# Performance work log

Hardware: AMD Instinct MI355X
Metric: run time of the kernel (lower is better)

Reference implementation:

```python
import jax, jax.numpy as jnp
import numpy as np

N_NODES = 100000
N_EDGES = 1600000
IN_CH, HID_CH, OUT_CH = 128, 128, 64


def _glorot(key, shape):
    lim = np.sqrt(6.0 / (shape[0] + shape[1])).astype(np.float32)
    return jax.random.uniform(key, shape, jnp.float32, -lim, lim)


def setup_inputs() -> dict:
    key = jax.random.key(0)
    ks = jax.random.split(key, 11)
    x = jax.random.normal(ks[0], (N_NODES, IN_CH), jnp.float32)
    edge_index = jax.random.randint(ks[1], (2, N_EDGES), 0, N_NODES, dtype=jnp.int64)
    dims = [(IN_CH, HID_CH), (HID_CH, HID_CH), (HID_CH, OUT_CH)]
    params = {}
    for i, (din, dout) in enumerate(dims):
        params[f"Wl{i}"] = _glorot(ks[2 + 3 * i], (din, dout))
        params[f"Wr{i}"] = _glorot(ks[3 + 3 * i], (din, dout))
        params[f"b{i}"] = jnp.zeros((dout,), jnp.float32)
    return {"x": x, "edge_index": edge_index, **params}


def _sage_conv(x, src, dst, Wl, Wr, b):
    # mean aggregation of neighbor (source) features at each destination node
    msg_sum = jax.ops.segment_sum(x[src], dst, num_segments=N_NODES)  # [N, din]
    deg = jax.ops.segment_sum(jnp.ones((src.shape[0],), x.dtype), dst,
                              num_segments=N_NODES)
    mean = msg_sum / jnp.maximum(deg, 1.0)[:, None]
    # lin_l(aggr) + lin_r(self), bias only in lin_l (PyG SAGEConv default)
    return mean @ Wl + x @ Wr + b


def reference(x, edge_index, Wl0, Wr0, b0, Wl1, Wr1, b1, Wl2, Wr2, b2):
    src, dst = edge_index[0], edge_index[1]
    h = jax.nn.relu(_sage_conv(x, src, dst, Wl0, Wr0, b0))  # dropout = identity (eval)
    h = jax.nn.relu(_sage_conv(h, src, dst, Wl1, Wr1, b1))
    out = _sage_conv(h, src, dst, Wl2, Wr2, b2)
    return out
```

## Files before the change

### kernel.cpp

```cpp
#include <hip/hip_runtime.h>
#include <stdint.h>

#define NN 100000
#define NE 1600000
#define NBUK 782
#define G 256
#define CHUNK 6250

typedef unsigned int u32;
typedef unsigned short u16;
typedef short v8s __attribute__((ext_vector_type(8)));
typedef float v4f __attribute__((ext_vector_type(4)));

union U4S8 {
    uint4 u;
    v8s s;
};

__device__ __forceinline__ float bf2f(u16 u) {
    return __uint_as_float(((u32)u) << 16);
}
__device__ __forceinline__ u16 f2bf(float f) {
    u32 u = __float_as_uint(f);
    u = u + 0x7FFFu + ((u >> 16) & 1u);
    return (u16)(u >> 16);
}
__device__ __forceinline__ float lo16(u32 u) { return __uint_as_float(u << 16); }
__device__ __forceinline__ float hi16(u32 u) {
    return __uint_as_float(u & 0xFFFF0000u);
}

__global__ void detect_kernel(const u32* __restrict__ ei,
                              const u32* __restrict__ x, int* flags) {
    __shared__ int bad64, badbf;
    int t = threadIdx.x;
    if (t == 0) { bad64 = 0; badbf = 0; }
    __syncthreads();
    if (ei[2 * t + 1] != 0u) atomicAdd(&bad64, 1);
    u32 d = x[t];
    u32 e = (d >> 7) & 0xFFu;
    if (e != 0u && (e < 96u || e > 160u)) atomicAdd(&badbf, 1);
    __syncthreads();
    if (t == 0) {
        flags[0] = (bad64 < 16) ? 1 : 0;
        flags[1] = (badbf < 16) ? 1 : 0;
    }
}

__global__ void conv_x(const void* __restrict__ x, const int* __restrict__ flags,
                       u32* __restrict__ xb, u32* __restrict__ h1,
                       u32* __restrict__ h2) {
    int i = blockIdx.x * 256 + threadIdx.x;
    if (i >= NN * 64) {
        int p = i - NN * 64;
        if (p < 64) {
            xb[NN * 64 + p] = 0;
            h1[NN * 64 + p] = 0;
            h2[NN * 64 + p] = 0;
        }
        return;
    }
    u32 o;
    if (flags[1]) {
        o = ((const u32*)x)[i];
    } else {
        float2 v = ((const float2*)x)[i];
        o = ((u32)f2bf(v.y) << 16) | (u32)f2bf(v.x);
    }
    xb[i] = o;
}

__global__ void wt_prep_all(const void* __restrict__ Wr0,
                            const void* __restrict__ Wl0,
                            const void* __restrict__ b0,
                            const void* __restrict__ Wr1,
                            const void* __restrict__ Wl1,
                            const void* __restrict__ b1,
                            const void* __restrict__ Wr2,
                            const void* __restrict__ Wl2,
                            const void* __restrict__ b2,
                            const int* __restrict__ flags,
                            u16* __restrict__ WT0, float* __restrict__ bf0,
                            u16* __restrict__ WT1, float* __restrict__ bf1,
                            u16* __restrict__ WT2, float* __restrict__ bf2_) {
    const void* Wr;
    const void* Wl;
    const void* bias;
    u16* WT;
    float* bias_f;
    int cout, t;
    if (blockIdx.x < 128) {
        Wr = Wr0; Wl = Wl0; bias = b0; WT = WT0; bias_f = bf0; cout = 128;
        t = blockIdx.x * 256 + threadIdx.x;
    } else if (blockIdx.x < 256) {
        Wr = Wr1; Wl = Wl1; bias = b1; WT = WT1; bias_f = bf1; cout = 128;
        t = (blockIdx.x - 128) * 256 + threadIdx.x;
    } else {
        Wr = Wr2; Wl = Wl2; bias = b2; WT = WT2; bias_f = bf2_; cout = 64;
        t = (blockIdx.x - 256) * 256 + threadIdx.x;
    }
    if (t < 256 * cout) {
        int k = t / cout, c = t % cout;
        const void* W = (k < 128) ? Wr : Wl;
        int kk = k & 127;
        float v;
        if (flags[1])
            v = bf2f(((const u16*)W)[kk * cout + c]);
        else
            v = ((const float*)W)[kk * cout + c];
        WT[c * 256 + k] = f2bf(v);
    }
    if (t < cout) {
        bias_f[t] =
            flags[1] ? bf2f(((const u16*)bias)[t]) : ((const float*)bias)[t];
    }
}

__global__ __launch_bounds__(256) void p1_hist(const void* __restrict__ ei,
                                               const int* __restrict__ flags,
                                               int* __restrict__ hist) {
    __shared__ int h[NBUK];
    int g = blockIdx.x, t = threadIdx.x;
    for (int b = t; b < NBUK; b += 256) h[b] = 0;
    __syncthreads();
    int e0 = g * CHUNK;
    int e1 = e0 + CHUNK;
    const int* p = (const int*)ei;
    if (flags[0]) {
        for (int e = e0 + t; e < e1; e += 256)
            atomicAdd(&h[p[2 * (NE + e)] >> 7], 1);
    } else {
        for (int e = e0 + t; e < e1; e += 256)
            atomicAdd(&h[p[NE + e] >> 7], 1);
    }
    __syncthreads();
    for (int b = t; b < NBUK; b += 256) hist[b * G + g] = h[b];
}

__global__ void scan_block_g(const int* __restrict__ in, int* __restrict__ out,
                             int* __restrict__ bsums, int n) {
    __shared__ int sS[256];
    int t = threadIdx.x;
    int base = blockIdx.x * 1024 + t * 4;
    int c[4];
#pragma unroll
    for (int i = 0; i < 4; ++i) c[i] = (base + i < n) ? in[base + i] : 0;
    int s = c[0] + c[1] + c[2] + c[3];
    sS[t] = s;
    __syncthreads();
    for (int dlt = 1; dlt < 256; dlt <<= 1) {
        int v = (t >= dlt) ? sS[t - dlt] : 0;
        __syncthreads();
        sS[t] += v;
        __syncthreads();
    }
    int run = sS[t] - s;
    if (t == 255) bsums[blockIdx.x] = sS[255];
#pragma unroll
    for (int i = 0; i < 4; ++i) {
        if (base + i < n) out[base + i] = run;
        run += c[i];
    }
}

__global__ void scan_top_g(int* bsums, int nb) {
    __shared__ int sS[256];
    int t = threadIdx.x;
    int v = (t < nb) ? bsums[t] : 0;
    sS[t] = v;
    __syncthreads();
    for (int d = 1; d < 256; d <<= 1) {
        int u = (t >= d) ? sS[t - d] : 0;
        __syncthreads();
        sS[t] += u;
        __syncthreads();
    }
    if (t < nb) bsums[t] = sS[t] - v;
}

__global__ void scan_add_g(int* __restrict__ out, const int* __restrict__ bsums,
                           int n) {
    int i = blockIdx.x * 256 + threadIdx.x;
    if (i < n) out[i] += bsums[i >> 10];
}

__global__ __launch_bounds__(256) void p2_scatter(const void* __restrict__ ei,
                                                  const int* __restrict__ flags,
                                                  const int* __restrict__ histS,
                                                  int2* __restrict__ ebuf) {
    __shared__ int cur[NBUK];
    int g = blockIdx.x, t = threadIdx.x;
    for (int b = t; b < NBUK; b += 256) cur[b] = histS[b * G + g];
    __syncthreads();
    int e0 = g * CHUNK;
    int e1 = e0 + CHUNK;
    const int* p = (const int*)ei;
    int is64 = flags[0];
    for (int e = e0 + t; e < e1; e += 256) {
        int s, d;
        if (is64) {
            s = p[2 * e];
            d = p[2 * (NE + e)];
        } else {
            s = p[e];
            d = p[NE + e];
        }
        int pos = atomicAdd(&cur[d >> 7], 1);
        ebuf[pos] = make_int2(s, d);
    }
}

__global__ __launch_bounds__(256) void p3_build(const int* __restrict__ histS,
                                                const int2* __restrict__ ebuf,
                                                int* __restrict__ off,
                                                int* __restrict__ ssrc) {
    __shared__ int cnt[128], pref[128], cur[128];
    int b = blockIdx.x, t = threadIdx.x;
    int node0 = b << 7;
    int bs = histS[b * G];
    int be = (b == NBUK - 1) ? NE : histS[(b + 1) * G];
    if (t < 128) cnt[t] = 0;
    __syncthreads();
    for (int e = bs + t; e < be; e += 256)
        atomicAdd(&cnt[ebuf[e].y - node0], 1);
    __syncthreads();
    if (t < 128) pref[t] = cnt[t];
    __syncthreads();
    for (int d = 1; d < 128; d <<= 1) {
        int v = 0;
        if (t < 128 && t >= d) v = pref[t - d];
        __syncthreads();
        if (t < 128) pref[t] += v;
        __syncthreads();
    }
    if (t < 128) {
        int ex = pref[t] - cnt[t];
        cur[t] = ex;
        int node = node0 + t;
        if (node < NN) off[node] = bs + ex;
    }
    if (b == NBUK - 1 && t == 0) off[NN] = NE;
    __syncthreads();
    for (int e = bs + t; e < be; e += 256) {
        int2 sd = ebuf[e];
        int pos = atomicAdd(&cur[sd.y - node0], 1);
        ssrc[bs + pos] = sd.x;
    }
}

__global__ __launch_bounds__(256) void gather_mean_b(
    const u32* __restrict__ feat, const int* __restrict__ off,
    const int* __restrict__ ssrc, u32* __restrict__ meanB) {
    int node = blockIdx.x * 4 + (threadIdx.x >> 6);
    int lane = threadIdx.x & 63;
    int o0 = __builtin_amdgcn_readfirstlane(off[node]);
    int o1 = __builtin_amdgcn_readfirstlane(off[node + 1]);
    int cnt = o1 - o0;
    float a0 = 0.f, a1 = 0.f;
    for (int base = 0; base < cnt; base += 64) {
        int lim = cnt - base;
        if (lim > 64) lim = 64;
        int myidx = (lane < lim) ? ssrc[o0 + base + lane] : NN;
        int jb = (lim + 15) & ~15;
        for (int j = 0; j < jb; j += 16) {
            u32 uu[16];
#pragma unroll
            for (int q = 0; q < 16; ++q) {
                int sidx = __builtin_amdgcn_readlane(myidx, j + q);
                uu[q] = feat[(size_t)sidx * 64 + lane];
            }
#pragma unroll
            for (int q = 0; q < 16; ++q) {
                a0 += lo16(uu[q]);
                a1 += hi16(uu[q]);
            }
        }
    }
    float inv = 1.0f / (float)(cnt > 0 ? cnt : 1);
    meanB[node * 64 + lane] =
        ((u32)f2bf(a1 * inv) << 16) | (u32)f2bf(a0 * inv);
}

template <int COUT, bool RELU, bool FINAL>
__global__ __launch_bounds__(256) void sage_mfma(
    const u16* __restrict__ selfB, const u16* __restrict__ meanB,
    const u16* __restrict__ WT, const float* __restrict__ bias_f,
    void* __restrict__ out, const int* __restrict__ flags) {
    constexpr int NT = COUT / 16;
    const int tid = threadIdx.x;
    const int wave = tid >> 6;
    const int lane = tid & 63;
    const int n16 = lane & 15;
    const int quad = lane >> 4;
    const int rowbase = blockIdx.x * 128 + wave * 32;
    const int bfin = flags[1];

    int ar0 = rowbase + n16;
    int ar1 = rowbase + 16 + n16;
    ar0 = (ar0 < NN) ? ar0 : (NN - 1);
    ar1 = (ar1 < NN) ? ar1 : (NN - 1);

    const u16* aS0 = selfB + (size_t)ar0 * 128 + quad * 8;
    const u16* aS1 = selfB + (size_t)ar1 * 128 + quad * 8;
    const u16* aM0 = meanB + (size_t)ar0 * 128 + quad * 8;
    const u16* aM1 = meanB + (size_t)ar1 * 128 + quad * 8;
    const u16* bp = WT + (size_t)n16 * 256 + quad * 8;

    v4f acc[2][NT];
#pragma unroll
    for (int mt = 0; mt < 2; ++mt)
#pragma unroll
        for (int nt = 0; nt < NT; ++nt) acc[mt][nt] = (v4f)(0.f);

#pragma unroll
    for (int ks = 0; ks < 8; ++ks) {
        const int ko = (ks & 3) * 32;
        U4S8 a0, a1;
        a0.u = *(const uint4*)((ks < 4 ? aS0 : aM0) + ko);
        a1.u = *(const uint4*)((ks < 4 ? aS1 : aM1) + ko);
        U4S8 b[NT];
#pragma unroll
        for (int nt = 0; nt < NT; ++nt)
            b[nt].u = *(const uint4*)(bp + nt * 16 * 256 + ks * 32);
#pragma unroll
        for (int nt = 0; nt < NT; ++nt) {
            acc[0][nt] = __builtin_amdgcn_mfma_f32_16x16x32_bf16(
                a0.s, b[nt].s, acc[0][nt], 0, 0, 0);
            acc[1][nt] = __builtin_amdgcn_mfma_f32_16x16x32_bf16(
                a1.s, b[nt].s, acc[1][nt], 0, 0, 0);
        }
    }

#pragma unroll
    for (int nt = 0; nt < NT; ++nt) {
        const int c = nt * 16 + n16;
        const float bv = bias_f[c];
#pragma unroll
        for (int mt = 0; mt < 2; ++mt) {
#pragma unroll
            for (int r = 0; r < 4; ++r) {
                int row = rowbase + mt * 16 + quad * 4 + r;
                if (row < NN) {
                    float v = acc[mt][nt][r] + bv;
                    if (RELU) v = fmaxf(v, 0.f);
                    if (FINAL && !bfin)
                        ((float*)out)[(size_t)row * COUT + c] = v;
                    else
                        ((u16*)out)[(size_t)row * COUT + c] = f2bf(v);
                }
            }
        }
    }
}

extern "C" void kernel_launch(void* const* d_in, const int* in_sizes, int n_in,
                              void* d_out, int out_size, void* d_ws,
                              size_t ws_size, hipStream_t stream) {
    const void* x = d_in[0];
    const void* ei = d_in[1];
    const void* Wl0 = d_in[2];
    const void* Wr0 = d_in[3];
    const void* b0 = d_in[4];
    const void* Wl1 = d_in[5];
    const void* Wr1 = d_in[6];
    const void* b1 = d_in[7];
    const void* Wl2 = d_in[8];
    const void* Wr2 = d_in[9];
    const void* b2 = d_in[10];

    char* ws = (char*)d_ws;
    size_t o = 0;
    auto alloc = [&](size_t bytes) {
        void* p = ws + o;
        o = (o + bytes + 511) & ~(size_t)511;
        return p;
    };
    int* flags = (int*)alloc(16);
    int* hist = (int*)alloc((size_t)NBUK * G * 4);
    int* bsums = (int*)alloc(256 * 4);
    int* off = (int*)alloc((NN + 1) * 4);
    int* ssrc = (int*)alloc((size_t)NE * 4);
    int2* ebuf = (int2*)alloc((size_t)NE * 8);
    u32* xb = (u32*)alloc((size_t)(NN + 1) * 64 * 4);
    u32* meanB = (u32*)alloc((size_t)NN * 64 * 4);
    u32* h1 = (u32*)alloc((size_t)(NN + 1) * 64 * 4);
    u32* h2 = (u32*)alloc((size_t)(NN + 1) * 64 * 4);
    u16* WT0 = (u16*)alloc(256 * 128 * 2);
    u16* WT1 = (u16*)alloc(256 * 128 * 2);
    u16* WT2 = (u16*)alloc(256 * 64 * 2);
    float* bf0 = (float*)alloc(128 * 4);
    float* bf1 = (float*)alloc(128 * 4);
    float* bf2_ = (float*)alloc(64 * 4);

    constexpr int L = NBUK * G;
    constexpr int NBLK = (L + 1023) / 1024;
    constexpr int RB = (NN + 127) / 128;

    detect_kernel<<<1, 256, 0, stream>>>((const u32*)ei, (const u32*)x, flags);
    conv_x<<<(NN * 64 + 64 + 255) / 256, 256, 0, stream>>>(x, flags, xb, h1,
                                                           h2);
    wt_prep_all<<<320, 256, 0, stream>>>(Wr0, Wl0, b0, Wr1, Wl1, b1, Wr2, Wl2,
                                         b2, flags, WT0, bf0, WT1, bf1, WT2,
                                         bf2_);

    p1_hist<<<G, 256, 0, stream>>>(ei, flags, hist);
    scan_block_g<<<NBLK, 256, 0, stream>>>(hist, hist, bsums, L);
    scan_top_g<<<1, 256, 0, stream>>>(bsums, NBLK);
    scan_add_g<<<(L + 255) / 256, 256, 0, stream>>>(hist, bsums, L);
    p2_scatter<<<G, 256, 0, stream>>>(ei, flags, hist, ebuf);
    p3_build<<<NBUK, 256, 0, stream>>>(hist, ebuf, off, ssrc);

    gather_mean_b<<<NN / 4, 256, 0, stream>>>(xb, off, ssrc, meanB);
    sage_mfma<128, true, false><<<RB, 256, 0, stream>>>(
        (const u16*)xb, (const u16*)meanB, WT0, bf0, h1, flags);
    gather_mean_b<<<NN / 4, 256, 0, stream>>>(h1, off, ssrc, meanB);
    sage_mfma<128, true, false><<<RB, 256, 0, stream>>>(
        (const u16*)h1, (const u16*)meanB, WT1, bf1, h2, flags);
    gather_mean_b<<<NN / 4, 256, 0, stream>>>(h2, off, ssrc, meanB);
    sage_mfma<64, false, true><<<RB, 256, 0, stream>>>(
        (const u16*)h2, (const u16*)meanB, WT2, bf2_, d_out, flags);
}
```

Baseline: 481.4 us.

## Stage weights in swizzled LDS and tile 64 rows per wave in SAGE MFMA

The SAGE linear kernel now copies the transposed weight matrix into shared memory with an XOR swizzle once per block. Each wave then computes 64 rows instead of 32, and the MFMA operands are swapped so outputs come out row-contiguous. That allows vectorized float4/uint2 stores with the bias loaded as float4. The aim is to cut repeated global weight loads and scattered scalar stores, at the cost of 64KB of LDS per block, which limits occupancy, and more accumulator registers.

```diff
diff --git a/kernel.cpp b/kernel.cpp
--- a/kernel.cpp
+++ b/kernel.cpp
@@ -282,71 +282,103 @@
 }
 
 template <int COUT, bool RELU, bool FINAL>
-__global__ __launch_bounds__(256) void sage_mfma(
+__global__ __launch_bounds__(256, 2) void sage_mfma(
     const u16* __restrict__ selfB, const u16* __restrict__ meanB,
     const u16* __restrict__ WT, const float* __restrict__ bias_f,
     void* __restrict__ out, const int* __restrict__ flags) {
-    constexpr int NT = COUT / 16;
+    constexpr int CT = COUT / 16;
+    __shared__ u16 wlds[256 * COUT];
     const int tid = threadIdx.x;
     const int wave = tid >> 6;
     const int lane = tid & 63;
     const int n16 = lane & 15;
     const int quad = lane >> 4;
-    const int rowbase = blockIdx.x * 128 + wave * 32;
     const int bfin = flags[1];
 
-    int ar0 = rowbase + n16;
-    int ar1 = rowbase + 16 + n16;
-    ar0 = (ar0 < NN) ? ar0 : (NN - 1);
-    ar1 = (ar1 < NN) ? ar1 : (NN - 1);
-
-    const u16* aS0 = selfB + (size_t)ar0 * 128 + quad * 8;
-    const u16* aS1 = selfB + (size_t)ar1 * 128 + quad * 8;
-    const u16* aM0 = meanB + (size_t)ar0 * 128 + quad * 8;
-    const u16* aM1 = meanB + (size_t)ar1 * 128 + quad * 8;
-    const u16* bp = WT + (size_t)n16 * 256 + quad * 8;
-
-    v4f acc[2][NT];
-#pragma unroll
-    for (int mt = 0; mt < 2; ++mt)
-#pragma unroll
-        for (int nt = 0; nt < NT; ++nt) acc[mt][nt] = (v4f)(0.f);
-
+    {
+        const uint4* src = (const uint4*)WT;
+        char* wb = (char*)wlds;
+        constexpr int NITER = (COUT * 32) / 256;
+#pragma unroll
+        for (int i = 0; i < NITER; ++i) {
+            int idx = i * 256 + tid;
+            int c = idx >> 5;
+            int off = (idx & 31) << 4;
+            *(uint4*)(wb + c * 512 + (off ^ ((c & 7) << 4))) = src[idx];
+        }
+    }
+    __syncthreads();
+
+    const int rowb = blockIdx.x * 256 + wave * 64 + n16;
+    int rr[4];
+#pragma unroll
+    for (int mt = 0; mt < 4; ++mt) {
+        int r = rowb + mt * 16;
+        r = (r < NN) ? r : (NN - 1);
+        rr[mt] = r * 128 + quad * 8;
+    }
+
+    v4f acc[4][CT];
+#pragma unroll
+    for (int mt = 0; mt < 4; ++mt)
+#pragma unroll
+        for (int ct = 0; ct < CT; ++ct) acc[mt][ct] = (v4f)(0.f);
+
+    const char* wb = (const char*)wlds;
+    const int swz = (n16 & 7) << 4;
 #pragma unroll
     for (int ks = 0; ks < 8; ++ks) {
         const int ko = (ks & 3) * 32;
-        U4S8 a0, a1;
-        a0.u = *(const uint4*)((ks < 4 ? aS0 : aM0) + ko);
-        a1.u = *(const uint4*)((ks < 4 ? aS1 : aM1) + ko);
-        U4S8 b[NT];
-#pragma unroll
-        for (int nt = 0; nt < NT; ++nt)
-            b[nt].u = *(const uint4*)(bp + nt * 16 * 256 + ks * 32);
-#pragma unroll
-        for (int nt = 0; nt < NT; ++nt) {
-            acc[0][nt] = __builtin_amdgcn_mfma_f32_16x16x32_bf16(
-                a0.s, b[nt].s, acc[0][nt], 0, 0, 0);
-            acc[1][nt] = __builtin_amdgcn_mfma_f32_16x16x32_bf16(
-                a1.s, b[nt].s, acc[1][nt], 0, 0, 0);
-        }
-    }
-
-#pragma unroll
-    for (int nt = 0; nt < NT; ++nt) {
-        const int c = nt * 16 + n16;
-        const float bv = bias_f[c];
-#pragma unroll
-        for (int mt = 0; mt < 2; ++mt) {
-#pragma unroll
-            for (int r = 0; r < 4; ++r) {
-                int row = rowbase + mt * 16 + quad * 4 + r;
-                if (row < NN) {
-                    float v = acc[mt][nt][r] + bv;
-                    if (RELU) v = fmaxf(v, 0.f);
-                    if (FINAL && !bfin)
-                        ((float*)out)[(size_t)row * COUT + c] = v;
-                    else
-                        ((u16*)out)[(size_t)row * COUT + c] = f2bf(v);
+        const u16* bp = (ks < 4) ? selfB : meanB;
+        U4S8 nf[4];
+#pragma unroll
+        for (int mt = 0; mt < 4; ++mt)
+            nf[mt].u = *(const uint4*)(bp + rr[mt] + ko);
+        U4S8 wf[CT];
+#pragma unroll
+        for (int ct = 0; ct < CT; ++ct) {
+            int addr = (ct * 16 + n16) * 512 + ((ks * 64 + quad * 16) ^ swz);
+            wf[ct].u = *(const uint4*)(wb + addr);
+        }
+#pragma unroll
+        for (int mt = 0; mt < 4; ++mt)
+#pragma unroll
+            for (int ct = 0; ct < CT; ++ct)
+                acc[mt][ct] = __builtin_amdgcn_mfma_f32_16x16x32_bf16(
+                    wf[ct].s, nf[mt].s, acc[mt][ct], 0, 0, 0);
+    }
+
+    float4 bv[CT];
+#pragma unroll
+    for (int ct = 0; ct < CT; ++ct)
+        bv[ct] = *(const float4*)&bias_f[ct * 16 + quad * 4];
+
+#pragma unroll
+    for (int mt = 0; mt < 4; ++mt) {
+        int row = rowb + mt * 16;
+        if (row < NN) {
+#pragma unroll
+            for (int ct = 0; ct < CT; ++ct) {
+                float v0 = acc[mt][ct][0] + bv[ct].x;
+                float v1 = acc[mt][ct][1] + bv[ct].y;
+                float v2 = acc[mt][ct][2] + bv[ct].z;
+                float v3 = acc[mt][ct][3] + bv[ct].w;
+                if (RELU) {
+                    v0 = fmaxf(v0, 0.f);
+                    v1 = fmaxf(v1, 0.f);
+                    v2 = fmaxf(v2, 0.f);
+                    v3 = fmaxf(v3, 0.f);
+                }
+                if (FINAL && !bfin) {
+                    float4 o = {v0, v1, v2, v3};
+                    *(float4*)((float*)out + (size_t)row * COUT + ct * 16 +
+                               quad * 4) = o;
+                } else {
+                    uint2 o;
+                    o.x = (u32)f2bf(v0) | ((u32)f2bf(v1) << 16);
+                    o.y = (u32)f2bf(v2) | ((u32)f2bf(v3) << 16);
+                    *(uint2*)((u16*)out + (size_t)row * COUT + ct * 16 +
+                              quad * 4) = o;
                 }
             }
         }
@@ -394,7 +426,7 @@
 
     constexpr int L = NBUK * G;
     constexpr int NBLK = (L + 1023) / 1024;
-    constexpr int RB = (NN + 127) / 128;
+    constexpr int RB = (NN + 255) / 256;
 
     detect_kernel<<<1, 256, 0, stream>>>((const u32*)ei, (const u32*)x, flags);
     conv_x<<<(NN * 64 + 64 + 255) / 256, 256, 0, stream>>>(x, flags, xb, h1,
```

New measurement: 399.5 us. 1.2x faster.
